# Kernel tuning notes

Hardware: AMD Instinct MI355X
Metric: run time of the kernel (lower is better)

Reference implementation:

```python
import jax, jax.numpy as jnp
import numpy as np

B, K, N = 8, 4, 131072
T = B * K * N  # upper bound on packed length
NEG_IDLE = -1e8   # logit value forced when slot is idle
NEG_FILL = -1000.0  # padded-output fill value for logits


def setup_inputs() -> dict:
    key = jax.random.key(0)
    k1, k2, k3, k4, k5, k6 = jax.random.split(key, 6)
    return {
        "rgb": jax.random.normal(k1, (T, 3), dtype=jnp.float32),
        "logits_surface": jax.random.normal(k2, (T, 1), dtype=jnp.float32),
        "logits_air": jax.random.normal(k3, (T, 1), dtype=jnp.float32),
        "mask_surface": jax.random.bernoulli(k4, 0.5, (B, K, N)),
        "mask_air": jax.random.bernoulli(k5, 0.5, (B, K, N)),
        "idle_states": jax.random.uniform(k6, (B, K), dtype=jnp.float32),
    }


def reference(rgb, logits_surface, logits_air, mask_surface, mask_air, idle_states):
    # Packed arrays are laid out in flattened (b, k, n) order: the packed index of a
    # masked element equals the count of True entries preceding it -> cumsum - 1.
    Bb, Kk, Nn = mask_surface.shape
    scale = (1.0 - idle_states)[:, :, None, None]          # [B,K,1,1]
    idle = idle_states[:, :, None, None]                   # [B,K,1,1]

    ms_flat = mask_surface.reshape(-1)
    idx_s = (jnp.cumsum(ms_flat.astype(jnp.int32)) - 1).reshape(Bb, Kk, Nn)
    ms = mask_surface[..., None]                           # [B,K,N,1]

    rgb_g = jnp.take(rgb, idx_s, axis=0)                   # [B,K,N,3]
    rgb_out = jnp.where(ms, rgb_g * scale, 0.0)

    ls_g = jnp.take(logits_surface, idx_s, axis=0)         # [B,K,N,1]
    logits_surface_out = jnp.where(ms, ls_g * scale + idle * NEG_IDLE, NEG_FILL)

    ma_flat = mask_air.reshape(-1)
    idx_a = (jnp.cumsum(ma_flat.astype(jnp.int32)) - 1).reshape(Bb, Kk, Nn)
    ma = mask_air[..., None]
    la_g = jnp.take(logits_air, idx_a, axis=0)             # [B,K,N,1]
    logits_air_out = jnp.where(ma, la_g * scale + idle * NEG_IDLE, NEG_FILL)

    return rgb_out, logits_surface_out, logits_air_out
```

## Files before the change

### kernel.cpp

```cpp
#include <hip/hip_runtime.h>
#include <stdint.h>

#define T_TOTAL  4194304
#define NEG_IDLE (-100000000.0f)
#define NEG_FILL (-1000.0f)

#define BLOCK  256
#define EPT    8
#define EPB    (BLOCK * EPT)
#define NCHUNK (T_TOTAL / EPB)


typedef unsigned u32x4 __attribute__((ext_vector_type(4)));

__device__ __forceinline__ unsigned decode8_i32(const u32x4* p) {
    const u32x4 a = __builtin_nontemporal_load(p);
    const u32x4 b = __builtin_nontemporal_load(p + 1);
    return (a.x ? 1u : 0u) | (a.y ? 2u : 0u) | (a.z ? 4u : 0u) | (a.w ? 8u : 0u)
         | (b.x ? 16u : 0u) | (b.y ? 32u : 0u) | (b.z ? 64u : 0u) | (b.w ? 128u : 0u);
}

__global__ __launch_bounds__(BLOCK) void reduce_pack_kernel(
    const u32x4* __restrict__ ms,
    const u32x4* __restrict__ ma,
    unsigned long long* __restrict__ sums,
    unsigned short* __restrict__ packed)
{
    const int blk  = blockIdx.x;
    const int tid  = threadIdx.x;
    const int lane = tid & 63;
    const int wave = tid >> 6;
    const size_t e = (size_t)blk * EPB + (size_t)tid * EPT;

    const unsigned bits_s = decode8_i32(ms + (e >> 2));
    const unsigned bits_a = decode8_i32(ma + (e >> 2));
    packed[blk * BLOCK + tid] = (unsigned short)(bits_s | (bits_a << 8));

    unsigned long long v =
        ((unsigned long long)(unsigned)__popc(bits_a) << 32) | (unsigned)__popc(bits_s);
    #pragma unroll
    for (int d = 32; d; d >>= 1) v += __shfl_down(v, d, 64);

    __shared__ unsigned long long w[BLOCK / 64];
    if (lane == 0) w[wave] = v;
    __syncthreads();
    if (tid == 0) sums[blk] = w[0] + w[1] + w[2] + w[3];
}

__global__ __launch_bounds__(BLOCK) void scatter_kernel(
    const float* __restrict__ rgb,
    const float* __restrict__ ls,
    const float* __restrict__ la,
    const unsigned long long* __restrict__ sums,
    const unsigned short* __restrict__ packed,
    const float* __restrict__ idle_states,
    float* __restrict__ out)
{
    const int bid  = blockIdx.x;
    const int role = bid >> 11;
    const int blk  = bid & (NCHUNK - 1);
    const int tid  = threadIdx.x;
    const int lane = tid & 63;
    const int wave = tid >> 6;
    const size_t base = (size_t)blk * EPB + (size_t)tid * EPT;

    const unsigned pw   = packed[blk * BLOCK + tid];
    const unsigned bits = (role == 2) ? (pw >> 8) : (pw & 0xffu);
    const int c = __popc(bits);

    unsigned long long acc = 0;
    {
        const ulonglong2* s2 = (const ulonglong2*)sums;
        const int i0 = tid * 8;
        #pragma unroll
        for (int q = 0; q < 4; ++q) {
            const ulonglong2 v = s2[tid * 4 + q];
            const int i = i0 + 2 * q;
            acc += (i     < blk) ? v.x : 0ull;
            acc += (i + 1 < blk) ? v.y : 0ull;
        }
        #pragma unroll
        for (int d = 32; d; d >>= 1) acc += __shfl_down(acc, d, 64);
    }

    int incl = c;
    #pragma unroll
    for (int d = 1; d < 64; d <<= 1) {
        const int t = __shfl_up(incl, d, 64);
        if (lane >= d) incl += t;
    }
    int excl = incl - c;

    __shared__ int wtot[BLOCK / 64];
    __shared__ unsigned long long wpre[BLOCK / 64];
    if (lane == 63) wtot[wave] = incl;
    if (lane == 0)  wpre[wave] = acc;
    __syncthreads();
    #pragma unroll
    for (int w = 0; w < BLOCK / 64; ++w)
        if (w < wave) excl += wtot[w];
    const unsigned long long pre = wpre[0] + wpre[1] + wpre[2] + wpre[3];
    const int pre32 = (role == 2) ? (int)(pre >> 32) : (int)(pre & 0xffffffffull);
    const int idx0  = pre32 + excl;

    int idx[EPT];
    #pragma unroll
    for (int j = 0; j < EPT; ++j)
        idx[j] = idx0 + __popc(bits & ((1u << j) - 1u));

    const float idle      = idle_states[blk >> 6];
    const float scale     = 1.0f - idle;
    const float idle_term = idle * NEG_IDLE;

    if (role == 0) {
        float r[3 * EPT];
        #pragma unroll
        for (int j = 0; j < EPT; ++j) {
            const float* rp = rgb + (size_t)idx[j] * 3;
            r[3 * j + 0] = rp[0];
            r[3 * j + 1] = rp[1];
            r[3 * j + 2] = rp[2];
        }
        #pragma unroll
        for (int j = 0; j < EPT; ++j) {
            const bool bs = (bits >> j) & 1u;
            r[3 * j + 0] = bs ? r[3 * j + 0] * scale : 0.0f;
            r[3 * j + 1] = bs ? r[3 * j + 1] * scale : 0.0f;
            r[3 * j + 2] = bs ? r[3 * j + 2] * scale : 0.0f;
        }
        float4* dst = (float4*)(out + base * 3);
        #pragma unroll
        for (int j = 0; j < 6; ++j) dst[j] = ((const float4*)r)[j];
    } else {
        const float* src = (role == 1) ? ls : la;
        float v[EPT];
        #pragma unroll
        for (int j = 0; j < EPT; ++j) v[j] = src[idx[j]];
        #pragma unroll
        for (int j = 0; j < EPT; ++j) {
            const bool b = (bits >> j) & 1u;
            v[j] = b ? (v[j] * scale + idle_term) : NEG_FILL;
        }
        float4* obase = (float4*)(out + (size_t)(2 + role) * T_TOTAL + base);
        obase[0] = ((const float4*)v)[0];
        obase[1] = ((const float4*)v)[1];
    }
}

extern "C" void kernel_launch(void* const* d_in, const int* in_sizes, int n_in,
                              void* d_out, int out_size, void* d_ws, size_t ws_size,
                              hipStream_t stream) {
    const float* rgb  = (const float*)d_in[0];
    const float* ls   = (const float*)d_in[1];
    const float* la   = (const float*)d_in[2];
    const u32x4* ms   = (const u32x4*)d_in[3];
    const u32x4* ma   = (const u32x4*)d_in[4];
    const float* idle = (const float*)d_in[5];
    float* out = (float*)d_out;

    unsigned long long* sums   = (unsigned long long*)d_ws;
    unsigned short*     packed =
        (unsigned short*)((uint8_t*)d_ws + NCHUNK * sizeof(unsigned long long));

    reduce_pack_kernel<<<NCHUNK, BLOCK, 0, stream>>>(ms, ma, sums, packed);
    scatter_kernel<<<3 * NCHUNK, BLOCK, 0, stream>>>(rgb, ls, la, sums, packed,
                                                     idle, out);
}
```

Measured before the change: 193.4 us.

## Add single-block prefix scan and stage contiguous source slices in LDS

Adds a separate scan kernel that computes exclusive prefixes of per-chunk counts once, so each scatter block no longer re-reads and reduces all 2048 chunk sums. The scatter kernel now loads its contiguous packed source slice (rgb/logits) coalesced into shared memory and gathers from LDS instead of issuing scattered global loads. This adds a kernel launch and 24KB of LDS per block, which may reduce occupancy.

```diff
diff --git a/kernel.cpp b/kernel.cpp
--- a/kernel.cpp
+++ b/kernel.cpp
@@ -10,6 +10,8 @@
 #define EPB    (BLOCK * EPT)
 #define NCHUNK (T_TOTAL / EPB)
 
+#define WS_PACKED_OFF  (NCHUNK * sizeof(unsigned long long))
+#define WS_PREFIX_OFF  (WS_PACKED_OFF + (size_t)NCHUNK * BLOCK * sizeof(unsigned short))
 
 typedef unsigned u32x4 __attribute__((ext_vector_type(4)));
 
@@ -47,15 +49,50 @@
     if (tid == 0) sums[blk] = w[0] + w[1] + w[2] + w[3];
 }
 
+__global__ __launch_bounds__(1024) void scan_kernel(
+    const unsigned long long* __restrict__ sums,
+    unsigned long long* __restrict__ prefix)
+{
+    const int tid  = threadIdx.x;
+    const int lane = tid & 63;
+    const int wave = tid >> 6;
+
+    const unsigned long long a = sums[2 * tid];
+    const unsigned long long b = sums[2 * tid + 1];
+    const unsigned long long s = a + b;
+
+    unsigned long long incl = s;
+    #pragma unroll
+    for (int d = 1; d < 64; d <<= 1) {
+        unsigned long long t = __shfl_up(incl, d, 64);
+        if (lane >= d) incl += t;
+    }
+
+    __shared__ unsigned long long wtot[16];
+    if (lane == 63) wtot[wave] = incl;
+    __syncthreads();
+    unsigned long long prior = 0;
+    #pragma unroll
+    for (int w = 0; w < 16; ++w)
+        if (w < wave) prior += wtot[w];
+
+    const unsigned long long excl = prior + (incl - s);
+    prefix[2 * tid]     = excl;
+    prefix[2 * tid + 1] = excl + a;
+}
+
 __global__ __launch_bounds__(BLOCK) void scatter_kernel(
     const float* __restrict__ rgb,
     const float* __restrict__ ls,
     const float* __restrict__ la,
-    const unsigned long long* __restrict__ sums,
+    const unsigned long long* __restrict__ prefix,
     const unsigned short* __restrict__ packed,
     const float* __restrict__ idle_states,
     float* __restrict__ out)
 {
+    __shared__ float stage[3 * EPB];
+    __shared__ int   wtot[BLOCK / 64];
+
     const int bid  = blockIdx.x;
     const int role = bid >> 11;
     const int blk  = bid & (NCHUNK - 1);
@@ -68,20 +105,8 @@
     const unsigned bits = (role == 2) ? (pw >> 8) : (pw & 0xffu);
     const int c = __popc(bits);
 
-    unsigned long long acc = 0;
-    {
-        const ulonglong2* s2 = (const ulonglong2*)sums;
-        const int i0 = tid * 8;
-        #pragma unroll
-        for (int q = 0; q < 4; ++q) {
-            const ulonglong2 v = s2[tid * 4 + q];
-            const int i = i0 + 2 * q;
-            acc += (i     < blk) ? v.x : 0ull;
-            acc += (i + 1 < blk) ? v.y : 0ull;
-        }
-        #pragma unroll
-        for (int d = 32; d; d >>= 1) acc += __shfl_down(acc, d, 64);
-    }
+    const unsigned long long pre64 = prefix[blk];
+    const int S0 = (role == 2) ? (int)(pre64 >> 32) : (int)(pre64 & 0xffffffffull);
 
     int incl = c;
     #pragma unroll
@@ -91,22 +116,27 @@
     }
     int excl = incl - c;
 
-    __shared__ int wtot[BLOCK / 64];
-    __shared__ unsigned long long wpre[BLOCK / 64];
     if (lane == 63) wtot[wave] = incl;
-    if (lane == 0)  wpre[wave] = acc;
     __syncthreads();
     #pragma unroll
     for (int w = 0; w < BLOCK / 64; ++w)
         if (w < wave) excl += wtot[w];
-    const unsigned long long pre = wpre[0] + wpre[1] + wpre[2] + wpre[3];
-    const int pre32 = (role == 2) ? (int)(pre >> 32) : (int)(pre & 0xffffffffull);
-    const int idx0  = pre32 + excl;
+    const int tot = wtot[0] + wtot[1] + wtot[2] + wtot[3];
 
-    int idx[EPT];
+    if (role == 0) {
+        const float* src = rgb + (size_t)3 * S0;
+        const int n = 3 * tot;
+        for (int i = tid; i < n; i += BLOCK) stage[i] = src[i];
+    } else {
+        const float* src = ((role == 1) ? ls : la) + S0;
+        for (int i = tid; i < tot; i += BLOCK) stage[i] = src[i];
+    }
+    __syncthreads();
+
+    int loc[EPT];
     #pragma unroll
     for (int j = 0; j < EPT; ++j)
-        idx[j] = idx0 + __popc(bits & ((1u << j) - 1u));
+        loc[j] = excl + __popc(bits & ((1u << j) - 1u));
 
     const float idle      = idle_states[blk >> 6];
     const float scale     = 1.0f - idle;
@@ -116,10 +146,9 @@
         float r[3 * EPT];
         #pragma unroll
         for (int j = 0; j < EPT; ++j) {
-            const float* rp = rgb + (size_t)idx[j] * 3;
-            r[3 * j + 0] = rp[0];
-            r[3 * j + 1] = rp[1];
-            r[3 * j + 2] = rp[2];
+            r[3 * j + 0] = stage[3 * loc[j] + 0];
+            r[3 * j + 1] = stage[3 * loc[j] + 1];
+            r[3 * j + 2] = stage[3 * loc[j] + 2];
         }
         #pragma unroll
         for (int j = 0; j < EPT; ++j) {
@@ -132,18 +161,17 @@
         #pragma unroll
         for (int j = 0; j < 6; ++j) dst[j] = ((const float4*)r)[j];
     } else {
-        const float* src = (role == 1) ? ls : la;
         float v[EPT];
         #pragma unroll
-        for (int j = 0; j < EPT; ++j) v[j] = src[idx[j]];
+        for (int j = 0; j < EPT; ++j) v[j] = stage[loc[j]];
         #pragma unroll
         for (int j = 0; j < EPT; ++j) {
             const bool b = (bits >> j) & 1u;
             v[j] = b ? (v[j] * scale + idle_term) : NEG_FILL;
         }
-        float4* obase = (float4*)(out + (size_t)(2 + role) * T_TOTAL + base);
-        obase[0] = ((const float4*)v)[0];
-        obase[1] = ((const float4*)v)[1];
+        float4* dst = (float4*)(out + (size_t)(2 + role) * T_TOTAL + base);
+        dst[0] = ((const float4*)v)[0];
+        dst[1] = ((const float4*)v)[1];
     }
 }
 
@@ -159,10 +187,11 @@
     float* out = (float*)d_out;
 
     unsigned long long* sums   = (unsigned long long*)d_ws;
-    unsigned short*     packed =
-        (unsigned short*)((uint8_t*)d_ws + NCHUNK * sizeof(unsigned long long));
+    unsigned short*     packed = (unsigned short*)((uint8_t*)d_ws + WS_PACKED_OFF);
+    unsigned long long* prefix = (unsigned long long*)((uint8_t*)d_ws + WS_PREFIX_OFF);
 
     reduce_pack_kernel<<<NCHUNK, BLOCK, 0, stream>>>(ms, ma, sums, packed);
-    scatter_kernel<<<3 * NCHUNK, BLOCK, 0, stream>>>(rgb, ls, la, sums, packed,
+    scan_kernel<<<1, 1024, 0, stream>>>(sums, prefix);
+    scatter_kernel<<<3 * NCHUNK, BLOCK, 0, stream>>>(rgb, ls, la, prefix, packed,
                                                      idle, out);
 }
```

Result: no change. 194.7 us (+0.7%).
